# Kernel optimization log

Measured on AMD Instinct MI355X. Metric: run time of the kernel, lower is better.

Reference implementation:

```python
import jax, jax.numpy as jnp
import numpy as np

NUM_HEADS = 16
LN_EPS = 1e-05


def setup_inputs() -> dict:
    key = jax.random.key(0)
    ks = jax.random.split(key, 10)
    B, S, H = 2, 2048, 1024
    s = 1.0 / np.sqrt(H)
    return {
        "hidden_states": jax.random.normal(ks[0], (B, S, H), dtype=jnp.float32),
        "Wq": jax.random.normal(ks[1], (H, H), dtype=jnp.float32) * s,
        "bq": jax.random.normal(ks[2], (H,), dtype=jnp.float32) * 0.02,
        "Wk": jax.random.normal(ks[3], (H, H), dtype=jnp.float32) * s,
        "bk": jax.random.normal(ks[4], (H,), dtype=jnp.float32) * 0.02,
        "Wv": jax.random.normal(ks[5], (H, H), dtype=jnp.float32) * s,
        "bv": jax.random.normal(ks[6], (H,), dtype=jnp.float32) * 0.02,
        "Wd": jax.random.normal(ks[7], (H, H), dtype=jnp.float32) * s,
        "bd": jax.random.normal(ks[8], (H,), dtype=jnp.float32) * 0.02,
        "ln_gamma": jnp.ones((H,), dtype=jnp.float32),
        "ln_beta": jnp.zeros((H,), dtype=jnp.float32),
    }


def reference(hidden_states, Wq, bq, Wk, bk, Wv, bv, Wd, bd, ln_gamma, ln_beta):
    B, S, H = hidden_states.shape
    nh = NUM_HEADS
    hd = H // nh

    # QKV projections (torch Linear: x @ W.T + b), split heads -> [B, nh, S, hd]
    def proj(W, b):
        y = jnp.einsum('bsh,oh->bso', hidden_states, W) + b
        return y.reshape(B, S, nh, hd).transpose(0, 2, 1, 3)

    q = proj(Wq, bq)
    k = proj(Wk, bk)
    v = proj(Wv, bv)

    # scaled dot-product attention: [B, nh, S, S]
    scores = jnp.einsum('bhqd,bhkd->bhqk', q, k) / jnp.sqrt(jnp.float32(hd))
    probs = jax.nn.softmax(scores, axis=-1)
    ctx = jnp.einsum('bhqk,bhkd->bhqd', probs, v)  # [B, nh, S, hd]
    ctx = ctx.transpose(0, 2, 1, 3).reshape(B, S, H)

    # output dense + residual + LayerNorm
    attn_out = jnp.einsum('bsh,oh->bso', ctx, Wd) + bd
    x = attn_out + hidden_states
    mu = jnp.mean(x, axis=-1, keepdims=True)
    var = jnp.mean(jnp.square(x - mu), axis=-1, keepdims=True)
    return (x - mu) * jax.lax.rsqrt(var + LN_EPS) * ln_gamma + ln_beta
```

## Files before the change

### kernel.cpp

```cpp
#include <hip/hip_runtime.h>

constexpr int kH    = 1024;
constexpr int kSEQ  = 2048;
constexpr int kBATCH= 2;
constexpr int kNH   = 16;
constexpr int kHD   = 64;
constexpr int kM    = 4096;
constexpr int kSPLIT= 4;
constexpr int kKEYS = kSEQ / kSPLIT;

typedef _Float16 h8  __attribute__((ext_vector_type(8)));
typedef _Float16 h4  __attribute__((ext_vector_type(4)));
typedef float   f32x4 __attribute__((ext_vector_type(4)));

static __device__ __forceinline__ f32x4 mfma16(h8 a, h8 b, f32x4 c) {
  return __builtin_amdgcn_mfma_f32_16x16x32_f16(a, b, c, 0, 0, 0);
}

static __device__ __forceinline__ void gll16(const _Float16* g, _Float16* l) {
  __builtin_amdgcn_global_load_lds(
      (const __attribute__((address_space(1))) void*)g,
      (__attribute__((address_space(3))) void*)l, 16, 0, 0);
}

#define QSCALE 0.18033688011112042f
#define C0INIT (-5.770780163555854f)

__global__ __launch_bounds__(256) void cvt_all(
    const float* __restrict__ X,  const float* __restrict__ Wq,
    const float* __restrict__ Wk, const float* __restrict__ Wv,
    const float* __restrict__ Wd,
    _Float16* __restrict__ Xh,  _Float16* __restrict__ Wqh,
    _Float16* __restrict__ Wkh, _Float16* __restrict__ Wvh,
    _Float16* __restrict__ Wdh)
{
  int i = blockIdx.x * 256 + threadIdx.x;
  const float* src; _Float16* dst; int off;
  if (i < (kM * kH) / 4) {
    src = X; dst = Xh; off = i;
  } else {
    int j = i - (kM * kH) / 4;
    int w = j >> 18;
    off = j & 262143;
    src = (w == 0) ? Wq : (w == 1) ? Wk : (w == 2) ? Wv : Wd;
    dst = (w == 0) ? Wqh : (w == 1) ? Wkh : (w == 2) ? Wvh : Wdh;
  }
  float4 v = reinterpret_cast<const float4*>(src)[off];
  h4 o;
  o[0] = (_Float16)v.x; o[1] = (_Float16)v.y;
  o[2] = (_Float16)v.z; o[3] = (_Float16)v.w;
  reinterpret_cast<h4*>(dst)[off] = o;
}

__global__ __launch_bounds__(256, 2) void qkv_gemm(
    const _Float16* __restrict__ Xh,
    const _Float16* __restrict__ Wq, const _Float16* __restrict__ Wk,
    const _Float16* __restrict__ Wv,
    const float* __restrict__ bq, const float* __restrict__ bk,
    const float* __restrict__ bv,
    _Float16* __restrict__ Qo, _Float16* __restrict__ Ko, _Float16* __restrict__ Vo)
{
  const int proj = blockIdx.z;
  const _Float16* W   = (proj == 0) ? Wq : ((proj == 1) ? Wk : Wv);
  const float*    bias= (proj == 0) ? bq : ((proj == 1) ? bk : bv);
  _Float16*       Out = (proj == 0) ? Qo : ((proj == 1) ? Ko : Vo);

  const int m0 = blockIdx.y * 128, n0 = blockIdx.x * 128;
  __shared__ __align__(16) _Float16 As[2][128 * 32];
  __shared__ __align__(16) _Float16 Bs[2][128 * 32];

  const int tid  = threadIdx.x;
  const int wave = tid >> 6, lane = tid & 63, quad = lane >> 4, l16 = lane & 15;
  const int mw = (wave & 1) * 64, nw = (wave >> 1) * 64;

  f32x4 acc[4][4] = {};
  const int grow = wave * 32 + (lane >> 2);
  const int gcol = (lane & 3) * 8;
  const _Float16* Ag = Xh + (size_t)(m0 + grow) * kH + gcol;
  const _Float16* Bg = W  + (size_t)(n0 + grow) * kH + gcol;

  {
    gll16(Ag,            &As[0][wave * 1024]);
    gll16(Ag + 16 * kH,  &As[0][wave * 1024 + 512]);
    gll16(Bg,            &Bs[0][wave * 1024]);
    gll16(Bg + 16 * kH,  &Bs[0][wave * 1024 + 512]);
  }

  for (int k = 0; k < 32; ++k) {
    const int cur = k & 1;
    __syncthreads();
    if (k < 31) {
      const int k0 = (k + 1) * 32, nb = cur ^ 1;
      gll16(Ag + k0,           &As[nb][wave * 1024]);
      gll16(Ag + 16 * kH + k0, &As[nb][wave * 1024 + 512]);
      gll16(Bg + k0,           &Bs[nb][wave * 1024]);
      gll16(Bg + 16 * kH + k0, &Bs[nb][wave * 1024 + 512]);
    }
    h8 af[4], bf[4];
    #pragma unroll
    for (int mi = 0; mi < 4; ++mi)
      af[mi] = *reinterpret_cast<const h8*>(&As[cur][(mw + mi * 16 + l16) * 32 + quad * 8]);
    #pragma unroll
    for (int ni = 0; ni < 4; ++ni)
      bf[ni] = *reinterpret_cast<const h8*>(&Bs[cur][(nw + ni * 16 + l16) * 32 + quad * 8]);
    #pragma unroll
    for (int mi = 0; mi < 4; ++mi)
      #pragma unroll
      for (int ni = 0; ni < 4; ++ni)
        acc[mi][ni] = mfma16(af[mi], bf[ni], acc[mi][ni]);
  }

  #pragma unroll
  for (int mi = 0; mi < 4; ++mi)
  #pragma unroll
  for (int ni = 0; ni < 4; ++ni) {
    const int ng = n0 + nw + ni * 16 + l16;
    const float bv_ = bias[ng];
    const int hh = ng >> 6, dd = ng & 63;
    #pragma unroll
    for (int r = 0; r < 4; ++r) {
      const int mg = m0 + mw + mi * 16 + quad * 4 + r;
      float val = acc[mi][ni][r] + bv_;
      if (proj == 0) val *= QSCALE;
      const int bb = mg >> 11, srow = mg & 2047;
      Out[(((size_t)(bb * kNH + hh) * kSEQ) + srow) * kHD + dd] = (_Float16)val;
    }
  }
}

__global__ __launch_bounds__(256) void vtrans(const _Float16* __restrict__ V,
                                              _Float16* __restrict__ Vt)
{
  const int st = blockIdx.x;
  const int bh = blockIdx.y;
  __shared__ __align__(16) _Float16 Lt[64][72];
  const int t = threadIdx.x, r = t >> 2, c = (t & 3) * 16;
  const _Float16* src = V + (size_t)bh * kSEQ * kHD + (size_t)(st * 64 + r) * kHD + c;
  h8 p0 = *reinterpret_cast<const h8*>(src);
  h8 p1 = *reinterpret_cast<const h8*>(src + 8);
  #pragma unroll
  for (int e = 0; e < 8; ++e) Lt[c + e][r] = p0[e];
  #pragma unroll
  for (int e = 0; e < 8; ++e) Lt[c + 8 + e][r] = p1[e];
  __syncthreads();
  _Float16* dst = Vt + (size_t)bh * kHD * kSEQ + (size_t)r * kSEQ + st * 64 + c;
  *reinterpret_cast<h8*>(dst)     = *reinterpret_cast<const h8*>(&Lt[r][c]);
  *reinterpret_cast<h8*>(dst + 8) = *reinterpret_cast<const h8*>(&Lt[r][c + 8]);
}

__global__ __launch_bounds__(128, 3) void attn_kernel(
    const _Float16* __restrict__ Q, const _Float16* __restrict__ K,
    const _Float16* __restrict__ Vt, _Float16* __restrict__ Op,
    float* __restrict__ lp)
{
  const int qt = blockIdx.x, bh = blockIdx.y, split = blockIdx.z;
  const int tid = threadIdx.x;
  const int wave = tid >> 6, lane = tid & 63, quad = lane >> 4, l16 = lane & 15;
  const int sw3 = l16 & 3, sw7 = l16 & 7;

  __shared__ __align__(16) _Float16 Kl[2][32 * 64];
  __shared__ __align__(16) _Float16 Vl[2][64 * 32];
  __shared__ __align__(16) _Float16 Pl[2][64 * 32];

  const _Float16* Qb = Q  + (size_t)bh * kSEQ * kHD;
  const _Float16* Kb = K  + (size_t)bh * kSEQ * kHD;
  const _Float16* Vb = Vt + (size_t)bh * kHD * kSEQ;
  const int soff = split * kKEYS;

  const int qbase = qt * 128 + wave * 64;
  h8 qf[4][2];
  #pragma unroll
  for (int qh = 0; qh < 4; ++qh)
    #pragma unroll
    for (int dh = 0; dh < 2; ++dh)
      qf[qh][dh] = *reinterpret_cast<const h8*>(
          &Qb[(size_t)(qbase + qh * 16 + l16) * kHD + dh * 32 + quad * 8]);

  const int krw = lane >> 3;
  const int kch = (lane & 7) ^ krw;
  const _Float16* Kg = Kb + (size_t)(soff + wave * 16 + krw) * kHD + kch * 8;
  const int vdl = lane >> 2;
  const int vch = (lane & 3) ^ (vdl & 3);
  const _Float16* Vg = Vb + (size_t)(wave * 32 + vdl) * kSEQ + soff + vch * 8;
  _Float16* PlW = Pl[wave];

  f32x4 o[4][4] = {};
  f32x4 ol[4] = {};
  h8 vones = {(_Float16)1.f, (_Float16)1.f, (_Float16)1.f, (_Float16)1.f,
              (_Float16)1.f, (_Float16)1.f, (_Float16)1.f, (_Float16)1.f};

  gll16(Kg,               &Kl[0][(wave * 16) * 64]);
  gll16(Kg + 8 * kHD,     &Kl[0][(wave * 16 + 8) * 64]);
  gll16(Vg,               &Vl[0][(wave * 32) * 32]);
  gll16(Vg + 16 * kSEQ,   &Vl[0][(wave * 32 + 16) * 32]);

  for (int kt = 0; kt < kKEYS / 32; ++kt) {
    const int cur = kt & 1;
    __syncthreads();
    if (kt + 1 < kKEYS / 32) {
      const int nb = cur ^ 1;
      const int ko = (kt + 1) * 32;
      gll16(Kg + (size_t)ko * kHD,            &Kl[nb][(wave * 16) * 64]);
      gll16(Kg + (size_t)(ko + 8) * kHD,      &Kl[nb][(wave * 16 + 8) * 64]);
      gll16(Vg + ko,                          &Vl[nb][(wave * 32) * 32]);
      gll16(Vg + 16 * kSEQ + ko,              &Vl[nb][(wave * 32 + 16) * 32]);
    }
    const _Float16* Kc = Kl[cur];
    const _Float16* Vc = Vl[cur];

    #pragma unroll
    for (int nt = 0; nt < 2; ++nt) {
      const int keyl = nt * 16 + l16;
      h8 ka0 = *reinterpret_cast<const h8*>(&Kc[keyl * 64 + ((quad     ) ^ sw7) * 8]);
      h8 ka1 = *reinterpret_cast<const h8*>(&Kc[keyl * 64 + ((quad ^ 4) ^ sw7) * 8]);
      #pragma unroll
      for (int qh = 0; qh < 4; ++qh) {
        f32x4 a = {C0INIT, C0INIT, C0INIT, C0INIT};
        a = mfma16(ka0, qf[qh][0], a);
        a = mfma16(ka1, qf[qh][1], a);
        h4 pp;
        pp[0] = (_Float16)exp2f(a[0]); pp[1] = (_Float16)exp2f(a[1]);
        pp[2] = (_Float16)exp2f(a[2]); pp[3] = (_Float16)exp2f(a[3]);
        const int row = qh * 16 + l16;
        const int c = (nt * 2 + (quad >> 1)) ^ sw3;
        *reinterpret_cast<h4*>(&PlW[row * 32 + c * 8 + (quad & 1) * 4]) = pp;
      }
    }
    h8 pa[4];
    #pragma unroll
    for (int qh = 0; qh < 4; ++qh)
      pa[qh] = *reinterpret_cast<const h8*>(
          &PlW[(qh * 16 + l16) * 32 + (quad ^ sw3) * 8]);
    #pragma unroll
    for (int dt = 0; dt < 4; ++dt) {
      h8 vb = *reinterpret_cast<const h8*>(
          &Vc[(dt * 16 + l16) * 32 + (quad ^ sw3) * 8]);
      #pragma unroll
      for (int qh = 0; qh < 4; ++qh)
        o[qh][dt] = mfma16(pa[qh], vb, o[qh][dt]);
    }
    #pragma unroll
    for (int qh = 0; qh < 4; ++qh)
      ol[qh] = mfma16(pa[qh], vones, ol[qh]);
  }

  const size_t pbase = ((size_t)(split * (kBATCH * kNH) + bh)) * kSEQ;
  #pragma unroll
  for (int qh = 0; qh < 4; ++qh)
    #pragma unroll
    for (int r = 0; r < 4; ++r) {
      const int qrow = qbase + qh * 16 + quad * 4 + r;
      if (l16 == 0) lp[pbase + qrow] = ol[qh][r];
      #pragma unroll
      for (int dt = 0; dt < 4; ++dt)
        Op[(pbase + qrow) * kHD + dt * 16 + l16] = (_Float16)o[qh][dt][r];
    }
}

__global__ __launch_bounds__(256) void attn_merge(
    const _Float16* __restrict__ Op, const float* __restrict__ lp,
    _Float16* __restrict__ Ctx)
{
  const int t = blockIdx.x * 256 + threadIdx.x;
  const int d8 = t & 7, q = (t >> 3) & (kSEQ - 1), bh = t >> 14;
  float acc[8] = {};
  float l = 0.f;
  #pragma unroll
  for (int s = 0; s < kSPLIT; ++s) {
    const size_t pbase = ((size_t)(s * (kBATCH * kNH) + bh)) * kSEQ + q;
    h8 v = *reinterpret_cast<const h8*>(&Op[pbase * kHD + d8 * 8]);
    #pragma unroll
    for (int e = 0; e < 8; ++e) acc[e] += (float)v[e];
    l += lp[pbase];
  }
  const float inv = 1.f / l;
  const int b = bh >> 4, hh = bh & 15;
  h8 ov;
  #pragma unroll
  for (int e = 0; e < 8; ++e) ov[e] = (_Float16)(acc[e] * inv);
  *reinterpret_cast<h8*>(&Ctx[((size_t)(b * kSEQ + q)) * kH + hh * kHD + d8 * 8]) = ov;
}

__global__ __launch_bounds__(256, 2) void dense_gemm(
    const _Float16* __restrict__ A, const _Float16* __restrict__ W,
    const float* __restrict__ bias, const float* __restrict__ resid,
    float* __restrict__ Out)
{
  const int m0 = blockIdx.y * 128, n0 = blockIdx.x * 128;
  __shared__ __align__(16) _Float16 As[2][128 * 32];
  __shared__ __align__(16) _Float16 Bs[2][128 * 32];
  const int tid  = threadIdx.x;
  const int wave = tid >> 6, lane = tid & 63, quad = lane >> 4, l16 = lane & 15;
  const int mw = (wave & 1) * 64, nw = (wave >> 1) * 64;
  f32x4 acc[4][4] = {};
  const int grow = wave * 32 + (lane >> 2);
  const int gcol = (lane & 3) * 8;
  const _Float16* Ag = A + (size_t)(m0 + grow) * kH + gcol;
  const _Float16* Bg = W + (size_t)(n0 + grow) * kH + gcol;

  {
    gll16(Ag,           &As[0][wave * 1024]);
    gll16(Ag + 16 * kH, &As[0][wave * 1024 + 512]);
    gll16(Bg,           &Bs[0][wave * 1024]);
    gll16(Bg + 16 * kH, &Bs[0][wave * 1024 + 512]);
  }

  for (int k = 0; k < 32; ++k) {
    const int cur = k & 1;
    __syncthreads();
    if (k < 31) {
      const int k0 = (k + 1) * 32, nb = cur ^ 1;
      gll16(Ag + k0,           &As[nb][wave * 1024]);
      gll16(Ag + 16 * kH + k0, &As[nb][wave * 1024 + 512]);
      gll16(Bg + k0,           &Bs[nb][wave * 1024]);
      gll16(Bg + 16 * kH + k0, &Bs[nb][wave * 1024 + 512]);
    }
    h8 af[4], bf[4];
    #pragma unroll
    for (int mi = 0; mi < 4; ++mi)
      af[mi] = *reinterpret_cast<const h8*>(&As[cur][(mw + mi * 16 + l16) * 32 + quad * 8]);
    #pragma unroll
    for (int ni = 0; ni < 4; ++ni)
      bf[ni] = *reinterpret_cast<const h8*>(&Bs[cur][(nw + ni * 16 + l16) * 32 + quad * 8]);
    #pragma unroll
    for (int mi = 0; mi < 4; ++mi)
      #pragma unroll
      for (int ni = 0; ni < 4; ++ni)
        acc[mi][ni] = mfma16(af[mi], bf[ni], acc[mi][ni]);
  }
  #pragma unroll
  for (int mi = 0; mi < 4; ++mi)
  #pragma unroll
  for (int ni = 0; ni < 4; ++ni) {
    const int ng = n0 + nw + ni * 16 + l16;
    const float bv_ = bias[ng];
    #pragma unroll
    for (int r = 0; r < 4; ++r) {
      const int mg = m0 + mw + mi * 16 + quad * 4 + r;
      Out[(size_t)mg * kH + ng] = acc[mi][ni][r] + bv_ + resid[(size_t)mg * kH + ng];
    }
  }
}

__global__ __launch_bounds__(256) void ln_kernel(const float* __restrict__ Tmp,
    const float* __restrict__ gamma, const float* __restrict__ beta,
    float* __restrict__ out)
{
  const int row = blockIdx.x;
  const float4 v = reinterpret_cast<const float4*>(Tmp + (size_t)row * kH)[threadIdx.x];
  float s  = v.x + v.y + v.z + v.w;
  float ss = v.x * v.x + v.y * v.y + v.z * v.z + v.w * v.w;
  #pragma unroll
  for (int off = 32; off > 0; off >>= 1) {
    s  += __shfl_down(s, off);
    ss += __shfl_down(ss, off);
  }
  __shared__ float red[8];
  const int wave = threadIdx.x >> 6, lane = threadIdx.x & 63;
  if (lane == 0) { red[wave] = s; red[4 + wave] = ss; }
  __syncthreads();
  s  = red[0] + red[1] + red[2] + red[3];
  ss = red[4] + red[5] + red[6] + red[7];
  const float mu   = s * (1.f / kH);
  const float var  = ss * (1.f / kH) - mu * mu;
  const float rstd = rsqrtf(var + 1e-5f);
  const float4 g  = reinterpret_cast<const float4*>(gamma)[threadIdx.x];
  const float4 bb = reinterpret_cast<const float4*>(beta)[threadIdx.x];
  float4 o;
  o.x = (v.x - mu) * rstd * g.x + bb.x;
  o.y = (v.y - mu) * rstd * g.y + bb.y;
  o.z = (v.z - mu) * rstd * g.z + bb.z;
  o.w = (v.w - mu) * rstd * g.w + bb.w;
  reinterpret_cast<float4*>(out + (size_t)row * kH)[threadIdx.x] = o;
}

extern "C" void kernel_launch(void* const* d_in, const int* in_sizes, int n_in,
                              void* d_out, int out_size, void* d_ws, size_t ws_size,
                              hipStream_t stream) {
  const float* hs    = (const float*)d_in[0];
  const float* Wq    = (const float*)d_in[1];
  const float* bq    = (const float*)d_in[2];
  const float* Wk    = (const float*)d_in[3];
  const float* bk    = (const float*)d_in[4];
  const float* Wv    = (const float*)d_in[5];
  const float* bv    = (const float*)d_in[6];
  const float* Wd    = (const float*)d_in[7];
  const float* bd    = (const float*)d_in[8];
  const float* gamma = (const float*)d_in[9];
  const float* beta  = (const float*)d_in[10];
  float* out = (float*)d_out;

  char* ws = (char*)d_ws;
  _Float16* Xh   = (_Float16*)(ws + 0);
  _Float16* Wqh  = (_Float16*)(ws + 8388608);
  _Float16* Wkh  = (_Float16*)(ws + 10485760);
  _Float16* Wvh  = (_Float16*)(ws + 12582912);
  _Float16* Wdh  = (_Float16*)(ws + 14680064);
  _Float16* Qh   = (_Float16*)(ws + 16777216);
  _Float16* Kh   = (_Float16*)(ws + 25165824);
  _Float16* Vh   = (_Float16*)(ws + 33554432);
  _Float16* Vtb  = Xh;
  float*    lpart= (float*)Wqh;
  _Float16* Opart= (_Float16*)(ws + 33554432);
  _Float16* Ctx  = Qh;
  float*    Tmp  = (float*)(ws + 50331648);

  cvt_all<<<8192, 256, 0, stream>>>(hs, Wq, Wk, Wv, Wd, Xh, Wqh, Wkh, Wvh, Wdh);
  qkv_gemm<<<dim3(kH / 128, kM / 128, 3), 256, 0, stream>>>(
      Xh, Wqh, Wkh, Wvh, bq, bk, bv, Qh, Kh, Vh);
  vtrans<<<dim3(kSEQ / 64, kBATCH * kNH), 256, 0, stream>>>(Vh, Vtb);
  attn_kernel<<<dim3(kSEQ / 128, kBATCH * kNH, kSPLIT), 128, 0, stream>>>(
      Qh, Kh, Vtb, Opart, lpart);
  attn_merge<<<2048, 256, 0, stream>>>(Opart, lpart, Ctx);
  dense_gemm<<<dim3(kH / 128, kM / 128), 256, 0, stream>>>(Ctx, Wdh, bd, hs, Tmp);
  ln_kernel<<<kM, 256, 0, stream>>>(Tmp, gamma, beta, out);
}
```

Measured before the change: 243.8 us.

## Use 32x32 MFMA for QK^T with 64-key tiles and in-register row sums

Reworks the attention kernel to compute scores with 32x32x16 MFMA over 64-key tiles instead of 16x16 MFMA over 32-key tiles. K and V tiles double in size in LDS. The softmax row sum is now accumulated from the fp32 exponentials in registers, replacing the extra MFMA against a ones vector. Occupancy hint drops from 3 to 2 blocks per CU because of the higher register and LDS use, which risks less latency hiding.

```diff
diff --git a/kernel.cpp b/kernel.cpp
--- a/kernel.cpp
+++ b/kernel.cpp
@@ -11,10 +11,14 @@
 
 typedef _Float16 h8  __attribute__((ext_vector_type(8)));
 typedef _Float16 h4  __attribute__((ext_vector_type(4)));
-typedef float   f32x4 __attribute__((ext_vector_type(4)));
+typedef float   f32x4  __attribute__((ext_vector_type(4)));
+typedef float   f32x16 __attribute__((ext_vector_type(16)));
 
 static __device__ __forceinline__ f32x4 mfma16(h8 a, h8 b, f32x4 c) {
   return __builtin_amdgcn_mfma_f32_16x16x32_f16(a, b, c, 0, 0, 0);
+}
+static __device__ __forceinline__ f32x16 mfma32(h8 a, h8 b, f32x16 c) {
+  return __builtin_amdgcn_mfma_f32_32x32x16_f16(a, b, c, 0, 0, 0);
 }
 
 static __device__ __forceinline__ void gll16(const _Float16* g, _Float16* l) {
@@ -148,112 +152,142 @@
   *reinterpret_cast<h8*>(dst + 8) = *reinterpret_cast<const h8*>(&Lt[r][c + 8]);
 }
 
-__global__ __launch_bounds__(128, 3) void attn_kernel(
+__global__ __launch_bounds__(128, 2) void attn_kernel(
     const _Float16* __restrict__ Q, const _Float16* __restrict__ K,
     const _Float16* __restrict__ Vt, _Float16* __restrict__ Op,
     float* __restrict__ lp)
 {
   const int qt = blockIdx.x, bh = blockIdx.y, split = blockIdx.z;
   const int tid = threadIdx.x;
-  const int wave = tid >> 6, lane = tid & 63, quad = lane >> 4, l16 = lane & 15;
-  const int sw3 = l16 & 3, sw7 = l16 & 7;
-
-  __shared__ __align__(16) _Float16 Kl[2][32 * 64];
-  __shared__ __align__(16) _Float16 Vl[2][64 * 32];
-  __shared__ __align__(16) _Float16 Pl[2][64 * 32];
+  const int wave = tid >> 6, lane = tid & 63;
+  const int quad = lane >> 4, l16 = lane & 15;
+  const int lane32 = lane & 31, half = lane >> 5;
+
+  __shared__ __align__(16) _Float16 Kl[2][64 * 64];
+  __shared__ __align__(16) _Float16 Vl[2][64 * 64];
+  __shared__ __align__(16) _Float16 Pl[2][32 * 64];
 
   const _Float16* Qb = Q  + (size_t)bh * kSEQ * kHD;
   const _Float16* Kb = K  + (size_t)bh * kSEQ * kHD;
   const _Float16* Vb = Vt + (size_t)bh * kHD * kSEQ;
   const int soff = split * kKEYS;
-
   const int qbase = qt * 128 + wave * 64;
-  h8 qf[4][2];
-  #pragma unroll
-  for (int qh = 0; qh < 4; ++qh)
-    #pragma unroll
-    for (int dh = 0; dh < 2; ++dh)
-      qf[qh][dh] = *reinterpret_cast<const h8*>(
-          &Qb[(size_t)(qbase + qh * 16 + l16) * kHD + dh * 32 + quad * 8]);
-
-  const int krw = lane >> 3;
-  const int kch = (lane & 7) ^ krw;
-  const _Float16* Kg = Kb + (size_t)(soff + wave * 16 + krw) * kHD + kch * 8;
-  const int vdl = lane >> 2;
-  const int vch = (lane & 3) ^ (vdl & 3);
-  const _Float16* Vg = Vb + (size_t)(wave * 32 + vdl) * kSEQ + soff + vch * 8;
-  _Float16* PlW = Pl[wave];
+
+  h8 qf[2][4];
+  #pragma unroll
+  for (int qc = 0; qc < 2; ++qc)
+    #pragma unroll
+    for (int kt = 0; kt < 4; ++kt)
+      qf[qc][kt] = *reinterpret_cast<const h8*>(
+          &Qb[(size_t)(qbase + qc * 32 + lane32) * kHD + kt * 16 + half * 8]);
+
+  const int srow = lane >> 3;
+  const int sch  = (lane & 7) ^ srow;
+  const _Float16* Kg = Kb + (size_t)(soff + wave * 32 + srow) * kHD + sch * 8;
+  const _Float16* Vg = Vb + (size_t)(wave * 32 + srow) * kSEQ + soff + sch * 8;
 
   f32x4 o[4][4] = {};
-  f32x4 ol[4] = {};
-  h8 vones = {(_Float16)1.f, (_Float16)1.f, (_Float16)1.f, (_Float16)1.f,
-              (_Float16)1.f, (_Float16)1.f, (_Float16)1.f, (_Float16)1.f};
-
-  gll16(Kg,               &Kl[0][(wave * 16) * 64]);
-  gll16(Kg + 8 * kHD,     &Kl[0][(wave * 16 + 8) * 64]);
-  gll16(Vg,               &Vl[0][(wave * 32) * 32]);
-  gll16(Vg + 16 * kSEQ,   &Vl[0][(wave * 32 + 16) * 32]);
-
-  for (int kt = 0; kt < kKEYS / 32; ++kt) {
+  float l_acc[2] = {0.f, 0.f};
+  f32x16 cinit;
+  #pragma unroll
+  for (int r = 0; r < 16; ++r) cinit[r] = C0INIT;
+
+  #pragma unroll
+  for (int i = 0; i < 4; ++i) {
+    gll16(Kg + i * 512,                 &Kl[0][(wave * 32 + i * 8) * 64]);
+    gll16(Vg + (size_t)i * 8 * kSEQ,    &Vl[0][(wave * 32 + i * 8) * 64]);
+  }
+
+  for (int kt = 0; kt < kKEYS / 64; ++kt) {
     const int cur = kt & 1;
     __syncthreads();
-    if (kt + 1 < kKEYS / 32) {
+    if (kt + 1 < kKEYS / 64) {
       const int nb = cur ^ 1;
-      const int ko = (kt + 1) * 32;
-      gll16(Kg + (size_t)ko * kHD,            &Kl[nb][(wave * 16) * 64]);
-      gll16(Kg + (size_t)(ko + 8) * kHD,      &Kl[nb][(wave * 16 + 8) * 64]);
-      gll16(Vg + ko,                          &Vl[nb][(wave * 32) * 32]);
-      gll16(Vg + 16 * kSEQ + ko,              &Vl[nb][(wave * 32 + 16) * 32]);
+      const int ko = (kt + 1) * 64;
+      #pragma unroll
+      for (int i = 0; i < 4; ++i) {
+        gll16(Kg + (size_t)ko * kHD + i * 512,        &Kl[nb][(wave * 32 + i * 8) * 64]);
+        gll16(Vg + (size_t)i * 8 * kSEQ + ko,         &Vl[nb][(wave * 32 + i * 8) * 64]);
+      }
     }
     const _Float16* Kc = Kl[cur];
     const _Float16* Vc = Vl[cur];
-
-    #pragma unroll
-    for (int nt = 0; nt < 2; ++nt) {
-      const int keyl = nt * 16 + l16;
-      h8 ka0 = *reinterpret_cast<const h8*>(&Kc[keyl * 64 + ((quad     ) ^ sw7) * 8]);
-      h8 ka1 = *reinterpret_cast<const h8*>(&Kc[keyl * 64 + ((quad ^ 4) ^ sw7) * 8]);
-      #pragma unroll
-      for (int qh = 0; qh < 4; ++qh) {
-        f32x4 a = {C0INIT, C0INIT, C0INIT, C0INIT};
-        a = mfma16(ka0, qf[qh][0], a);
-        a = mfma16(ka1, qf[qh][1], a);
-        h4 pp;
-        pp[0] = (_Float16)exp2f(a[0]); pp[1] = (_Float16)exp2f(a[1]);
-        pp[2] = (_Float16)exp2f(a[2]); pp[3] = (_Float16)exp2f(a[3]);
-        const int row = qh * 16 + l16;
-        const int c = (nt * 2 + (quad >> 1)) ^ sw3;
-        *reinterpret_cast<h4*>(&PlW[row * 32 + c * 8 + (quad & 1) * 4]) = pp;
+    _Float16* PlW = Pl[wave];
+
+    h8 ka[2][4];
+    #pragma unroll
+    for (int kc = 0; kc < 2; ++kc)
+      #pragma unroll
+      for (int dt = 0; dt < 4; ++dt)
+        ka[kc][dt] = *reinterpret_cast<const h8*>(
+            &Kc[(kc * 32 + lane32) * 64 + (((dt * 2 + half) ^ (lane32 & 7)) * 8)]);
+    h8 vbf[4][2];
+    #pragma unroll
+    for (int dt = 0; dt < 4; ++dt)
+      #pragma unroll
+      for (int kc = 0; kc < 2; ++kc)
+        vbf[dt][kc] = *reinterpret_cast<const h8*>(
+            &Vc[(dt * 16 + l16) * 64 + (((kc * 4 + quad) ^ (l16 & 7)) * 8)]);
+
+    #pragma unroll
+    for (int qc = 0; qc < 2; ++qc) {
+      f32x16 s0 = cinit, s1 = cinit;
+      #pragma unroll
+      for (int dt = 0; dt < 4; ++dt) s0 = mfma32(ka[0][dt], qf[qc][dt], s0);
+      #pragma unroll
+      for (int dt = 0; dt < 4; ++dt) s1 = mfma32(ka[1][dt], qf[qc][dt], s1);
+
+      float la = 0.f;
+      #pragma unroll
+      for (int kc = 0; kc < 2; ++kc) {
+        const f32x16& sv = kc ? s1 : s0;
+        #pragma unroll
+        for (int g = 0; g < 4; ++g) {
+          float e0 = exp2f(sv[4 * g + 0]);
+          float e1 = exp2f(sv[4 * g + 1]);
+          float e2 = exp2f(sv[4 * g + 2]);
+          float e3 = exp2f(sv[4 * g + 3]);
+          la += (e0 + e1) + (e2 + e3);
+          h4 pp;
+          pp[0] = (_Float16)e0; pp[1] = (_Float16)e1;
+          pp[2] = (_Float16)e2; pp[3] = (_Float16)e3;
+          *reinterpret_cast<h4*>(
+              &PlW[lane32 * 64 + (((kc * 4 + g) ^ (lane32 & 7)) * 8) + half * 4]) = pp;
+        }
       }
-    }
-    h8 pa[4];
-    #pragma unroll
-    for (int qh = 0; qh < 4; ++qh)
-      pa[qh] = *reinterpret_cast<const h8*>(
-          &PlW[(qh * 16 + l16) * 32 + (quad ^ sw3) * 8]);
-    #pragma unroll
-    for (int dt = 0; dt < 4; ++dt) {
-      h8 vb = *reinterpret_cast<const h8*>(
-          &Vc[(dt * 16 + l16) * 32 + (quad ^ sw3) * 8]);
-      #pragma unroll
-      for (int qh = 0; qh < 4; ++qh)
-        o[qh][dt] = mfma16(pa[qh], vb, o[qh][dt]);
-    }
-    #pragma unroll
-    for (int qh = 0; qh < 4; ++qh)
-      ol[qh] = mfma16(pa[qh], vones, ol[qh]);
+      l_acc[qc] += la;
+
+      h8 pa[2][2];
+      #pragma unroll
+      for (int qh = 0; qh < 2; ++qh)
+        #pragma unroll
+        for (int kc = 0; kc < 2; ++kc)
+          pa[qh][kc] = *reinterpret_cast<const h8*>(
+              &PlW[(qh * 16 + l16) * 64 + (((kc * 4 + quad) ^ (l16 & 7)) * 8)]);
+      #pragma unroll
+      for (int qh = 0; qh < 2; ++qh)
+        #pragma unroll
+        for (int dt = 0; dt < 4; ++dt) {
+          o[qc * 2 + qh][dt] = mfma16(pa[qh][0], vbf[dt][0], o[qc * 2 + qh][dt]);
+          o[qc * 2 + qh][dt] = mfma16(pa[qh][1], vbf[dt][1], o[qc * 2 + qh][dt]);
+        }
+    }
   }
 
   const size_t pbase = ((size_t)(split * (kBATCH * kNH) + bh)) * kSEQ;
   #pragma unroll
+  for (int qc = 0; qc < 2; ++qc) {
+    l_acc[qc] += __shfl_xor(l_acc[qc], 32);
+    if (half == 0) lp[pbase + qbase + qc * 32 + lane32] = l_acc[qc];
+  }
+  #pragma unroll
   for (int qh = 0; qh < 4; ++qh)
     #pragma unroll
     for (int r = 0; r < 4; ++r) {
-      const int qrow = qbase + qh * 16 + quad * 4 + r;
-      if (l16 == 0) lp[pbase + qrow] = ol[qh][r];
+      const int q = qbase + qh * 16 + quad * 4 + r;
       #pragma unroll
       for (int dt = 0; dt < 4; ++dt)
-        Op[(pbase + qrow) * kHD + dt * 16 + l16] = (_Float16)o[qh][dt][r];
+        Op[(pbase + q) * kHD + dt * 16 + l16] = (_Float16)o[qh][dt][r];
     }
 }
 
```

Result: faster. 234.7 us (-3.8%).
